# Kernel tuning notes

Hardware: AMD Instinct MI355X
Metric: run time of the kernel (lower is better)

The kernel has to match this reference:

```python
import jax, jax.numpy as jnp
import numpy as np

NUM_EMBEDDINGS = 1024
LATENT_SIZE = 256
N = 131072


def setup_inputs() -> dict:
    key = jax.random.key(0)
    k1, k2 = jax.random.split(key)
    inputs = jax.random.normal(k1, (N, LATENT_SIZE), dtype=jnp.float32)
    embed = jax.random.normal(k2, (LATENT_SIZE, NUM_EMBEDDINGS), dtype=jnp.float32)
    return {"inputs": inputs, "embed": embed}


def reference(inputs, embed):
    # Squared Euclidean distances: [N, K]
    dist = (
        jnp.sum(inputs * inputs, axis=1, keepdims=True)
        - 2.0 * (inputs @ embed)
        + jnp.sum(embed * embed, axis=0, keepdims=True)
    )
    embed_ind = jnp.argmin(dist, axis=1)  # [N]
    embed_onehot = jax.nn.one_hot(embed_ind, NUM_EMBEDDINGS, dtype=inputs.dtype)  # [N, K]
    # Gather codebook vectors: embedding lookup into embed.T -> [N, D]
    quantize = embed.T[embed_ind]
    # Commitment-style loss (eval path: no EMA buffer updates)
    loss = jnp.mean((jax.lax.stop_gradient(quantize) - inputs) ** 2)
    # Straight-through estimator
    quantize = inputs + jax.lax.stop_gradient(quantize - inputs)
    avg_probs = jnp.mean(embed_onehot, axis=0)  # [K]
    perplexity = jnp.exp(-jnp.sum(avg_probs * jnp.log(avg_probs + 1e-10)))
    return quantize, loss, perplexity, embed_ind
```

## Files before the change

kernel.cpp:

```cpp
#include <hip/hip_runtime.h>
#include <math.h>

#define M_ROWS 131072
#define D_DIM 256
#define NCODES 1024
#define QELEMS (M_ROWS * D_DIM)

typedef __attribute__((ext_vector_type(4))) short short4v;
typedef __attribute__((ext_vector_type(8))) short short8v;
typedef __attribute__((ext_vector_type(4))) float f32x4;

#define WS_EMBEDT   0u
#define WS_EHI      1048576u
#define WS_ELO      1572864u
#define WS_ENORM    2097152u
#define WS_PART     2101248u
#define WS_IDX2     18878464u
#define WS_COUNTS   19927040u
#define WS_LOSSP    19931136u

__device__ inline unsigned short f2bf(float x) {
  union { float f; unsigned u; } c; c.f = x;
  unsigned u = c.u;
  u += 0x7FFFu + ((u >> 16) & 1u);
  return (unsigned short)(u >> 16);
}
__device__ inline float bf2f(unsigned short h) {
  union { float f; unsigned u; } c; c.u = ((unsigned)h) << 16;
  return c.f;
}
__device__ inline void merge2(float& b0, int& i0, float& b1, int& i1,
                              float o0, int oi0, float o1, int oi1) {
  if (o0 < b0 || (o0 == b0 && oi0 < i0)) {
    if (b0 < o1 || (b0 == o1 && i0 < oi1)) { b1 = b0; i1 = i0; }
    else { b1 = o1; i1 = oi1; }
    b0 = o0; i0 = oi0;
  } else {
    if (o0 < b1 || (o0 == b1 && oi0 < i1)) { b1 = o0; i1 = oi0; }
  }
}

__global__ __launch_bounds__(256) void k_prep(const float* __restrict__ embed,
                                              float* __restrict__ embedT,
                                              unsigned short* __restrict__ ehiT,
                                              unsigned short* __restrict__ eloT,
                                              float* __restrict__ enorm) {
  int c = blockIdx.x, t = threadIdx.x;
  float v = embed[t * NCODES + c];
  embedT[c * D_DIM + t] = v;
  unsigned short hi = f2bf(v);
  ehiT[c * D_DIM + t] = hi;
  eloT[c * D_DIM + t] = f2bf(v - bf2f(hi));
  float s = v * v;
  for (int off = 32; off > 0; off >>= 1) s += __shfl_down(s, off, 64);
  __shared__ float red[4];
  if ((t & 63) == 0) red[t >> 6] = s;
  __syncthreads();
  if (t == 0) enorm[c] = red[0] + red[1] + red[2] + red[3];
}

__global__ __launch_bounds__(256, 3) void k_dist(const float* __restrict__ A,
                                                 const unsigned short* __restrict__ ehiT,
                                                 const unsigned short* __restrict__ eloT,
                                                 const float* __restrict__ enorm,
                                                 float4* __restrict__ partials) {
  __shared__ unsigned short sAhi[128 * 32];
  __shared__ unsigned short sAlo[128 * 32];
  __shared__ unsigned short sBhi[128 * 32];
  __shared__ unsigned short sBlo[128 * 32];
  __shared__ float4 sRed[2][128];

  int bx = blockIdx.x;
  int ct = bx & 7, rt = bx >> 3;
  int rowBase = rt << 7, colBase = ct << 7;
  int t = threadIdx.x;
  int w = t >> 6, lane = t & 63;
  int wr = w >> 1, wc = w & 1;
  int lm = lane & 15, quad = lane >> 4;

  int sr = t >> 1;
  int skh = (t & 1) << 4;

  f32x4 acc[4][4];
#pragma unroll
  for (int i = 0; i < 4; ++i)
#pragma unroll
    for (int j = 0; j < 4; ++j) acc[i][j] = (f32x4){0.f, 0.f, 0.f, 0.f};

  int aoff[4], boff[4];
#pragma unroll
  for (int ti = 0; ti < 4; ++ti) {
    int r = (wr << 6) + (ti << 4) + lm;
    aoff[ti] = r * 32 + ((quad ^ (r & 3)) << 3);
    int n = (wc << 6) + (ti << 4) + lm;
    boff[ti] = n * 32 + ((quad ^ (n & 3)) << 3);
  }

  const float* Arow = A + (size_t)(rowBase + sr) * D_DIM + skh;
  const unsigned short* Bhirow = ehiT + (size_t)(colBase + sr) * D_DIM + skh;
  const unsigned short* Blorow = eloT + (size_t)(colBase + sr) * D_DIM + skh;

  for (int kc = 0; kc < D_DIM; kc += 32) {
#pragma unroll
    for (int u = 0; u < 4; ++u) {
      float4 v = *(const float4*)(Arow + kc + (u << 2));
      int koff = skh + (u << 2);
      int dst = sr * 32 + (((koff >> 3) ^ (sr & 3)) << 3) + (koff & 7);
      unsigned short h0 = f2bf(v.x), h1 = f2bf(v.y), h2 = f2bf(v.z), h3 = f2bf(v.w);
      short4v hv = {(short)h0, (short)h1, (short)h2, (short)h3};
      *(short4v*)&sAhi[dst] = hv;
      short4v lv = {(short)f2bf(v.x - bf2f(h0)), (short)f2bf(v.y - bf2f(h1)),
                    (short)f2bf(v.z - bf2f(h2)), (short)f2bf(v.w - bf2f(h3))};
      *(short4v*)&sAlo[dst] = lv;
    }
#pragma unroll
    for (int h = 0; h < 2; ++h) {
      int koff = skh + (h << 3);
      int dst = sr * 32 + (((koff >> 3) ^ (sr & 3)) << 3);
      *(uint4*)&sBhi[dst] = *(const uint4*)(Bhirow + kc + (h << 3));
      *(uint4*)&sBlo[dst] = *(const uint4*)(Blorow + kc + (h << 3));
    }
    __syncthreads();

    short8v ahi[4], alo[4], bhi[4], blo[4];
#pragma unroll
    for (int i = 0; i < 4; ++i) {
      ahi[i] = *(const short8v*)&sAhi[aoff[i]];
      bhi[i] = *(const short8v*)&sBhi[boff[i]];
      blo[i] = *(const short8v*)&sBlo[boff[i]];
      alo[i] = *(const short8v*)&sAlo[aoff[i]];
    }
#pragma unroll
    for (int i = 0; i < 4; ++i)
#pragma unroll
      for (int j = 0; j < 4; ++j)
        acc[i][j] = __builtin_amdgcn_mfma_f32_16x16x32_bf16(ahi[i], bhi[j], acc[i][j], 0, 0, 0);
#pragma unroll
    for (int i = 0; i < 4; ++i)
#pragma unroll
      for (int j = 0; j < 4; ++j)
        acc[i][j] = __builtin_amdgcn_mfma_f32_16x16x32_bf16(ahi[i], blo[j], acc[i][j], 0, 0, 0);
#pragma unroll
    for (int i = 0; i < 4; ++i)
#pragma unroll
      for (int j = 0; j < 4; ++j)
        acc[i][j] = __builtin_amdgcn_mfma_f32_16x16x32_bf16(alo[i], bhi[j], acc[i][j], 0, 0, 0);
    __syncthreads();
  }

  float enC[4]; int cidx[4];
#pragma unroll
  for (int j = 0; j < 4; ++j) {
    cidx[j] = colBase + (wc << 6) + (j << 4) + lm;
    enC[j] = enorm[cidx[j]];
  }
#pragma unroll
  for (int ti = 0; ti < 4; ++ti) {
#pragma unroll
    for (int reg = 0; reg < 4; ++reg) {
      float b0 = 3.0e38f, b1 = 3.0e38f;
      int i0 = 0x7fffffff, i1 = 0x7fffffff;
#pragma unroll
      for (int j = 0; j < 4; ++j) {
        float v = fmaf(-2.f, acc[ti][j][reg], enC[j]);
        int c = cidx[j];
        if (v < b0 || (v == b0 && c < i0)) { b1 = b0; i1 = i0; b0 = v; i0 = c; }
        else if (v < b1 || (v == b1 && c < i1)) { b1 = v; i1 = c; }
      }
      for (int m = 1; m < 16; m <<= 1) {
        float o0 = __shfl_xor(b0, m, 64); int oi0 = __shfl_xor(i0, m, 64);
        float o1 = __shfl_xor(b1, m, 64); int oi1 = __shfl_xor(i1, m, 64);
        merge2(b0, i0, b1, i1, o0, oi0, o1, oi1);
      }
      if (lm == 0) {
        int rloc = (wr << 6) + (ti << 4) + (quad << 2) + reg;
        sRed[wc][rloc] = make_float4(b0, (float)i0, b1, (float)i1);
      }
    }
  }
  __syncthreads();
  if (t < 128) {
    float4 p = sRed[0][t];
    float b0 = p.x; int i0 = (int)p.y; float b1 = p.z; int i1 = (int)p.w;
    float4 q = sRed[1][t];
    merge2(b0, i0, b1, i1, q.x, (int)q.y, q.z, (int)q.w);
    partials[(size_t)ct * M_ROWS + rowBase + t] = make_float4(b0, (float)i0, b1, (float)i1);
  }
}

__global__ __launch_bounds__(256) void k_argmin(const float4* __restrict__ partials,
                                                int2* __restrict__ idx2) {
  int row = blockIdx.x * 256 + threadIdx.x;
  float b0 = 3.0e38f, b1 = 3.0e38f;
  int i0 = 0x7fffffff, i1 = 0x7fffffff;
#pragma unroll
  for (int tp = 0; tp < 8; ++tp) {
    float4 p = partials[(size_t)tp * M_ROWS + row];
    merge2(b0, i0, b1, i1, p.x, (int)p.y, p.z, (int)p.w);
  }
  idx2[row] = make_int2(i0, i1);
}

__global__ __launch_bounds__(256) void k_quant(const float* __restrict__ x,
                                               const float* __restrict__ embedT,
                                               const int2* __restrict__ idx2,
                                               float* __restrict__ outq,
                                               float* __restrict__ out_ind,
                                               int* __restrict__ counts,
                                               float* __restrict__ lossPart) {
  int b = blockIdx.x, t = threadIdx.x;
  int rl = t >> 6, lane = t & 63;
  float lsum = 0.f;
  __shared__ float red[4];
#pragma unroll
  for (int ri = 0; ri < 4; ++ri) {
    int row = b * 16 + ri * 4 + rl;
    int2 cc = idx2[row];
    float4 xv = *(const float4*)(x + (size_t)row * D_DIM + (lane << 2));
    float4 q0 = *(const float4*)(embedT + (size_t)cc.x * D_DIM + (lane << 2));
    float4 q1 = *(const float4*)(embedT + (size_t)cc.y * D_DIM + (lane << 2));
    float a0 = q0.x - xv.x, a1 = q0.y - xv.y, a2 = q0.z - xv.z, a3 = q0.w - xv.w;
    float c0 = q1.x - xv.x, c1 = q1.y - xv.y, c2 = q1.z - xv.z, c3 = q1.w - xv.w;
    float d0 = fmaf(a0, a0, fmaf(a1, a1, fmaf(a2, a2, a3 * a3)));
    float d1 = fmaf(c0, c0, fmaf(c1, c1, fmaf(c2, c2, c3 * c3)));
    for (int m = 1; m < 64; m <<= 1) {
      d0 += __shfl_xor(d0, m, 64);
      d1 += __shfl_xor(d1, m, 64);
    }
    bool sel = (d1 < d0) || (d1 == d0 && cc.y < cc.x);
    int widx = sel ? cc.y : cc.x;
    float4 qv;
    qv.x = sel ? q1.x : q0.x; qv.y = sel ? q1.y : q0.y;
    qv.z = sel ? q1.z : q0.z; qv.w = sel ? q1.w : q0.w;
    float4 o = make_float4(xv.x + (qv.x - xv.x), xv.y + (qv.y - xv.y),
                           xv.z + (qv.z - xv.z), xv.w + (qv.w - xv.w));
    *(float4*)(outq + (size_t)row * D_DIM + (lane << 2)) = o;
    lsum += sel ? d1 : d0;
    if (lane == 0) {
      out_ind[row] = (float)widx;
      atomicAdd(&counts[widx], 1);
    }
  }
  if (lane == 0) red[rl] = lsum;
  __syncthreads();
  if (t == 0) lossPart[b] = red[0] + red[1] + red[2] + red[3];
}

__global__ __launch_bounds__(1024) void k_final(const int* __restrict__ counts,
                                                const float* __restrict__ lossPart,
                                                float* __restrict__ out_scalars) {
  int t = threadIdx.x;
  double ls = 0.0;
#pragma unroll
  for (int u = 0; u < 8; ++u) ls += (double)lossPart[t * 8 + u];
  float p = (float)counts[t] * (1.0f / (float)M_ROWS);
  float ent = p * logf(p + 1e-10f);
  double lred = ls;
  float ered = ent;
  for (int off = 32; off > 0; off >>= 1) {
    lred += __shfl_down(lred, off, 64);
    ered += __shfl_down(ered, off, 64);
  }
  __shared__ double lsh[16];
  __shared__ float esh[16];
  int w = t >> 6;
  if ((t & 63) == 0) { lsh[w] = lred; esh[w] = ered; }
  __syncthreads();
  if (t == 0) {
    double L = 0.0;
    float E = 0.f;
    for (int i = 0; i < 16; ++i) { L += lsh[i]; E += esh[i]; }
    out_scalars[0] = (float)(L / (double)QELEMS);
    out_scalars[1] = expf(-E);
  }
}

extern "C" void kernel_launch(void* const* d_in, const int* in_sizes, int n_in,
                              void* d_out, int out_size, void* d_ws, size_t ws_size,
                              hipStream_t stream) {
  const float* inputs = (const float*)d_in[0];
  const float* embed = (const float*)d_in[1];
  float* out = (float*)d_out;
  char* ws = (char*)d_ws;
  float* embedT = (float*)(ws + WS_EMBEDT);
  unsigned short* ehiT = (unsigned short*)(ws + WS_EHI);
  unsigned short* eloT = (unsigned short*)(ws + WS_ELO);
  float* enorm = (float*)(ws + WS_ENORM);
  float4* partials = (float4*)(ws + WS_PART);
  int2* idx2 = (int2*)(ws + WS_IDX2);
  int* counts = (int*)(ws + WS_COUNTS);
  float* lossPart = (float*)(ws + WS_LOSSP);

  hipMemsetAsync(counts, 0, NCODES * sizeof(int), stream);
  k_prep<<<NCODES, 256, 0, stream>>>(embed, embedT, ehiT, eloT, enorm);
  k_dist<<<8192, 256, 0, stream>>>(inputs, ehiT, eloT, enorm, partials);
  k_argmin<<<M_ROWS / 256, 256, 0, stream>>>(partials, idx2);
  k_quant<<<8192, 256, 0, stream>>>(inputs, embedT, idx2, out, out + QELEMS + 2,
                                    counts, lossPart);
  k_final<<<1, 1024, 0, stream>>>(counts, lossPart, out + QELEMS);
}
```

Before: 972.5 us.

## Pre-split inputs to bf16 hi/lo tiles and stream via global_load_lds

Adds a pass that splits the fp32 inputs once into swizzled, tile-contiguous bf16 hi/lo buffers. The embedding split is stored in the same tiled layout, so the distance kernel can copy tiles straight into LDS with global_load_lds instead of redoing the conversion in each of the 8 column-tile blocks per row tile. It also remaps block indices so blocks sharing a row tile land on the same XCD, interleaves LDS fragment loads with MFMA groups, and switches rounding to truncation. This costs an extra pass writing about 134MB of workspace, and it only runs when the workspace is large enough; otherwise the old path is kept.

Measured after the change: 924.3 us. 4.9% less time.

```diff
diff --git a/kernel.cpp b/kernel.cpp
--- a/kernel.cpp
+++ b/kernel.cpp
@@ -6,29 +6,40 @@
 #define NCODES 1024
 #define QELEMS (M_ROWS * D_DIM)
 
-typedef __attribute__((ext_vector_type(4))) short short4v;
 typedef __attribute__((ext_vector_type(8))) short short8v;
 typedef __attribute__((ext_vector_type(4))) float f32x4;
-
-#define WS_EMBEDT   0u
-#define WS_EHI      1048576u
-#define WS_ELO      1572864u
-#define WS_ENORM    2097152u
-#define WS_PART     2101248u
-#define WS_IDX2     18878464u
-#define WS_COUNTS   19927040u
-#define WS_LOSSP    19931136u
-
-__device__ inline unsigned short f2bf(float x) {
-  union { float f; unsigned u; } c; c.f = x;
-  unsigned u = c.u;
-  u += 0x7FFFu + ((u >> 16) & 1u);
-  return (unsigned short)(u >> 16);
-}
-__device__ inline float bf2f(unsigned short h) {
-  union { float f; unsigned u; } c; c.u = ((unsigned)h) << 16;
-  return c.f;
-}
+typedef unsigned short ushort_t;
+
+#define WS_EMBEDT 0u
+#define WS_B1     1048576u
+#define WS_B2     1572864u
+#define WS_ENORM  2097152u
+#define WS_PART   2101248u
+#define WS_IDX2   18878464u
+#define WS_COUNTS 19927040u
+#define WS_LOSSP  19931136u
+#define WS_XHI    19963904u
+#define WS_XLO    87072768u
+#define WS_FAST_TOTAL 154181632u
+
+typedef unsigned int u32_g __attribute__((address_space(1)));
+typedef unsigned int u32_l __attribute__((address_space(3)));
+__device__ inline void gll16(const void* g, void* l) {
+  __builtin_amdgcn_global_load_lds((const u32_g*)g, (u32_l*)l, 16, 0, 0);
+}
+
+__device__ inline unsigned pack2(float x, float y) {
+  return __builtin_amdgcn_perm(__float_as_uint(y), __float_as_uint(x), 0x07060302u);
+}
+__device__ inline float rem1(float x) {
+  return x - __uint_as_float(__float_as_uint(x) & 0xFFFF0000u);
+}
+__device__ inline void split8(float4 a, float4 b, uint4* hi, uint4* lo) {
+  *hi = make_uint4(pack2(a.x, a.y), pack2(a.z, a.w), pack2(b.x, b.y), pack2(b.z, b.w));
+  *lo = make_uint4(pack2(rem1(a.x), rem1(a.y)), pack2(rem1(a.z), rem1(a.w)),
+                   pack2(rem1(b.x), rem1(b.y)), pack2(rem1(b.z), rem1(b.w)));
+}
+
 __device__ inline void merge2(float& b0, int& i0, float& b1, int& i1,
                               float o0, int oi0, float o1, int oi1) {
   if (o0 < b0 || (o0 == b0 && oi0 < i0)) {
@@ -42,15 +53,23 @@
 
 __global__ __launch_bounds__(256) void k_prep(const float* __restrict__ embed,
                                               float* __restrict__ embedT,
-                                              unsigned short* __restrict__ ehiT,
-                                              unsigned short* __restrict__ eloT,
-                                              float* __restrict__ enorm) {
+                                              ushort_t* __restrict__ b1,
+                                              ushort_t* __restrict__ b2,
+                                              float* __restrict__ enorm, int fast) {
   int c = blockIdx.x, t = threadIdx.x;
   float v = embed[t * NCODES + c];
   embedT[c * D_DIM + t] = v;
-  unsigned short hi = f2bf(v);
-  ehiT[c * D_DIM + t] = hi;
-  eloT[c * D_DIM + t] = f2bf(v - bf2f(hi));
+  unsigned bits = __float_as_uint(v);
+  ushort_t hi = (ushort_t)(bits >> 16);
+  ushort_t lo = (ushort_t)(__float_as_uint(rem1(v)) >> 16);
+  if (fast) {
+    int ct = c >> 7, cl = c & 127, kc = t >> 5, u = (t >> 3) & 3, j = t & 7;
+    size_t off = (size_t)(ct * 8 + kc) * 4096 + cl * 32 + ((u ^ (cl & 3)) << 3) + j;
+    b1[off] = hi; b2[off] = lo;
+  } else {
+    b1[c * D_DIM + t] = hi;
+    b2[c * D_DIM + t] = lo;
+  }
   float s = v * v;
   for (int off = 32; off > 0; off >>= 1) s += __shfl_down(s, off, 64);
   __shared__ float red[4];
@@ -59,95 +78,37 @@
   if (t == 0) enorm[c] = red[0] + red[1] + red[2] + red[3];
 }
 
-__global__ __launch_bounds__(256, 3) void k_dist(const float* __restrict__ A,
-                                                 const unsigned short* __restrict__ ehiT,
-                                                 const unsigned short* __restrict__ eloT,
-                                                 const float* __restrict__ enorm,
-                                                 float4* __restrict__ partials) {
-  __shared__ unsigned short sAhi[128 * 32];
-  __shared__ unsigned short sAlo[128 * 32];
-  __shared__ unsigned short sBhi[128 * 32];
-  __shared__ unsigned short sBlo[128 * 32];
-  __shared__ float4 sRed[2][128];
-
-  int bx = blockIdx.x;
-  int ct = bx & 7, rt = bx >> 3;
-  int rowBase = rt << 7, colBase = ct << 7;
-  int t = threadIdx.x;
-  int w = t >> 6, lane = t & 63;
-  int wr = w >> 1, wc = w & 1;
-  int lm = lane & 15, quad = lane >> 4;
-
+__global__ __launch_bounds__(256) void k_asplit(const float* __restrict__ x,
+                                                ushort_t* __restrict__ xhi,
+                                                ushort_t* __restrict__ xlo) {
+  int rt = blockIdx.x, t = threadIdx.x;
   int sr = t >> 1;
-  int skh = (t & 1) << 4;
-
-  f32x4 acc[4][4];
-#pragma unroll
-  for (int i = 0; i < 4; ++i)
-#pragma unroll
-    for (int j = 0; j < 4; ++j) acc[i][j] = (f32x4){0.f, 0.f, 0.f, 0.f};
-
-  int aoff[4], boff[4];
-#pragma unroll
-  for (int ti = 0; ti < 4; ++ti) {
-    int r = (wr << 6) + (ti << 4) + lm;
-    aoff[ti] = r * 32 + ((quad ^ (r & 3)) << 3);
-    int n = (wc << 6) + (ti << 4) + lm;
-    boff[ti] = n * 32 + ((quad ^ (n & 3)) << 3);
-  }
-
-  const float* Arow = A + (size_t)(rowBase + sr) * D_DIM + skh;
-  const unsigned short* Bhirow = ehiT + (size_t)(colBase + sr) * D_DIM + skh;
-  const unsigned short* Blorow = eloT + (size_t)(colBase + sr) * D_DIM + skh;
-
-  for (int kc = 0; kc < D_DIM; kc += 32) {
-#pragma unroll
-    for (int u = 0; u < 4; ++u) {
-      float4 v = *(const float4*)(Arow + kc + (u << 2));
-      int koff = skh + (u << 2);
-      int dst = sr * 32 + (((koff >> 3) ^ (sr & 3)) << 3) + (koff & 7);
-      unsigned short h0 = f2bf(v.x), h1 = f2bf(v.y), h2 = f2bf(v.z), h3 = f2bf(v.w);
-      short4v hv = {(short)h0, (short)h1, (short)h2, (short)h3};
-      *(short4v*)&sAhi[dst] = hv;
-      short4v lv = {(short)f2bf(v.x - bf2f(h0)), (short)f2bf(v.y - bf2f(h1)),
-                    (short)f2bf(v.z - bf2f(h2)), (short)f2bf(v.w - bf2f(h3))};
-      *(short4v*)&sAlo[dst] = lv;
-    }
-#pragma unroll
-    for (int h = 0; h < 2; ++h) {
-      int koff = skh + (h << 3);
-      int dst = sr * 32 + (((koff >> 3) ^ (sr & 3)) << 3);
-      *(uint4*)&sBhi[dst] = *(const uint4*)(Bhirow + kc + (h << 3));
-      *(uint4*)&sBlo[dst] = *(const uint4*)(Blorow + kc + (h << 3));
-    }
-    __syncthreads();
-
-    short8v ahi[4], alo[4], bhi[4], blo[4];
-#pragma unroll
-    for (int i = 0; i < 4; ++i) {
-      ahi[i] = *(const short8v*)&sAhi[aoff[i]];
-      bhi[i] = *(const short8v*)&sBhi[boff[i]];
-      blo[i] = *(const short8v*)&sBlo[boff[i]];
-      alo[i] = *(const short8v*)&sAlo[aoff[i]];
-    }
-#pragma unroll
-    for (int i = 0; i < 4; ++i)
-#pragma unroll
-      for (int j = 0; j < 4; ++j)
-        acc[i][j] = __builtin_amdgcn_mfma_f32_16x16x32_bf16(ahi[i], bhi[j], acc[i][j], 0, 0, 0);
-#pragma unroll
-    for (int i = 0; i < 4; ++i)
-#pragma unroll
-      for (int j = 0; j < 4; ++j)
-        acc[i][j] = __builtin_amdgcn_mfma_f32_16x16x32_bf16(ahi[i], blo[j], acc[i][j], 0, 0, 0);
-#pragma unroll
-    for (int i = 0; i < 4; ++i)
-#pragma unroll
-      for (int j = 0; j < 4; ++j)
-        acc[i][j] = __builtin_amdgcn_mfma_f32_16x16x32_bf16(alo[i], bhi[j], acc[i][j], 0, 0, 0);
-    __syncthreads();
-  }
-
+  int kh = (t & 1) << 4;
+  int s3 = sr & 3;
+  const float* row = x + ((size_t)(rt << 7) + sr) * D_DIM + kh;
+  size_t tb = (size_t)rt * 32768;
+#pragma unroll
+  for (int kc = 0; kc < 8; ++kc) {
+    float4 v0 = *(const float4*)(row + kc * 32 + 0);
+    float4 v1 = *(const float4*)(row + kc * 32 + 4);
+    float4 v2 = *(const float4*)(row + kc * 32 + 8);
+    float4 v3 = *(const float4*)(row + kc * 32 + 12);
+    uint4 h0, l0, h1, l1;
+    split8(v0, v1, &h0, &l0);
+    split8(v2, v3, &h1, &l1);
+    int u0 = kh >> 3;
+    size_t base = tb + (size_t)kc * 4096 + sr * 32;
+    *(uint4*)&xhi[base + ((u0 ^ s3) << 3)] = h0;
+    *(uint4*)&xhi[base + (((u0 + 1) ^ s3) << 3)] = h1;
+    *(uint4*)&xlo[base + ((u0 ^ s3) << 3)] = l0;
+    *(uint4*)&xlo[base + (((u0 + 1) ^ s3) << 3)] = l1;
+  }
+}
+
+__device__ inline void dist_epilogue(f32x4 (&acc)[4][4], const float* __restrict__ enorm,
+                                     float4* __restrict__ partials, float4 (*sRed)[128],
+                                     int t, int wr, int wc, int lm, int quad,
+                                     int rowBase, int colBase, int ct) {
   float enC[4]; int cidx[4];
 #pragma unroll
   for (int j = 0; j < 4; ++j) {
@@ -188,6 +149,176 @@
   }
 }
 
+__global__ __launch_bounds__(256, 3) void k_dist_fast(const ushort_t* __restrict__ xhi,
+                                                      const ushort_t* __restrict__ xlo,
+                                                      const ushort_t* __restrict__ bhi,
+                                                      const ushort_t* __restrict__ blo,
+                                                      const float* __restrict__ enorm,
+                                                      float4* __restrict__ partials) {
+  __shared__ ushort_t sAhi[4096], sAlo[4096], sBhi[4096], sBlo[4096];
+  __shared__ float4 sRed[2][128];
+
+  int bx = blockIdx.x;
+  int xcd = bx & 7, slot = bx >> 3;
+  int rt = (xcd << 7) | (slot >> 3);
+  int ct = slot & 7;
+  int rowBase = rt << 7, colBase = ct << 7;
+  int t = threadIdx.x;
+  int w = t >> 6, lane = t & 63;
+  int wr = w >> 1, wc = w & 1;
+  int lm = lane & 15, quad = lane >> 4;
+
+  f32x4 acc[4][4];
+#pragma unroll
+  for (int i = 0; i < 4; ++i)
+#pragma unroll
+    for (int j = 0; j < 4; ++j) acc[i][j] = (f32x4){0.f, 0.f, 0.f, 0.f};
+
+  int aoff[4], boff[4];
+#pragma unroll
+  for (int ti = 0; ti < 4; ++ti) {
+    int r = (wr << 6) + (ti << 4) + lm;
+    aoff[ti] = r * 32 + ((quad ^ (r & 3)) << 3);
+    int n = (wc << 6) + (ti << 4) + lm;
+    boff[ti] = n * 32 + ((quad ^ (n & 3)) << 3);
+  }
+
+  int c0 = w << 1;
+  int src0 = c0 * 512 + lane * 8;
+  const ushort_t* gA = xhi + (size_t)rt * 32768;
+  const ushort_t* gAl = xlo + (size_t)rt * 32768;
+  const ushort_t* gB = bhi + (size_t)ct * 32768;
+  const ushort_t* gBl = blo + (size_t)ct * 32768;
+
+  for (int kc = 0; kc < 8; ++kc) {
+    int src = kc * 4096 + src0;
+    gll16(gA + src, &sAhi[c0 * 512]);
+    gll16(gA + src + 512, &sAhi[(c0 + 1) * 512]);
+    gll16(gAl + src, &sAlo[c0 * 512]);
+    gll16(gAl + src + 512, &sAlo[(c0 + 1) * 512]);
+    gll16(gB + src, &sBhi[c0 * 512]);
+    gll16(gB + src + 512, &sBhi[(c0 + 1) * 512]);
+    gll16(gBl + src, &sBlo[c0 * 512]);
+    gll16(gBl + src + 512, &sBlo[(c0 + 1) * 512]);
+    __syncthreads();
+
+    short8v ahi[4], bhi_f[4];
+#pragma unroll
+    for (int i = 0; i < 4; ++i) {
+      ahi[i] = *(const short8v*)&sAhi[aoff[i]];
+      bhi_f[i] = *(const short8v*)&sBhi[boff[i]];
+    }
+#pragma unroll
+    for (int i = 0; i < 4; ++i)
+#pragma unroll
+      for (int j = 0; j < 4; ++j)
+        acc[i][j] = __builtin_amdgcn_mfma_f32_16x16x32_bf16(ahi[i], bhi_f[j], acc[i][j], 0, 0, 0);
+    short8v blo_f[4];
+#pragma unroll
+    for (int i = 0; i < 4; ++i) blo_f[i] = *(const short8v*)&sBlo[boff[i]];
+#pragma unroll
+    for (int i = 0; i < 4; ++i)
+#pragma unroll
+      for (int j = 0; j < 4; ++j)
+        acc[i][j] = __builtin_amdgcn_mfma_f32_16x16x32_bf16(ahi[i], blo_f[j], acc[i][j], 0, 0, 0);
+    short8v alo[4];
+#pragma unroll
+    for (int i = 0; i < 4; ++i) alo[i] = *(const short8v*)&sAlo[aoff[i]];
+#pragma unroll
+    for (int i = 0; i < 4; ++i)
+#pragma unroll
+      for (int j = 0; j < 4; ++j)
+        acc[i][j] = __builtin_amdgcn_mfma_f32_16x16x32_bf16(alo[i], bhi_f[j], acc[i][j], 0, 0, 0);
+    __syncthreads();
+  }
+
+  dist_epilogue(acc, enorm, partials, sRed, t, wr, wc, lm, quad, rowBase, colBase, ct);
+}
+
+__global__ __launch_bounds__(256, 3) void k_dist_slow(const float* __restrict__ A,
+                                                      const ushort_t* __restrict__ ehiT,
+                                                      const ushort_t* __restrict__ eloT,
+                                                      const float* __restrict__ enorm,
+                                                      float4* __restrict__ partials) {
+  __shared__ ushort_t sAhi[4096], sAlo[4096], sBhi[4096], sBlo[4096];
+  __shared__ float4 sRed[2][128];
+
+  int bx = blockIdx.x;
+  int ct = bx & 7, rt = bx >> 3;
+  int rowBase = rt << 7, colBase = ct << 7;
+  int t = threadIdx.x;
+  int w = t >> 6, lane = t & 63;
+  int wr = w >> 1, wc = w & 1;
+  int lm = lane & 15, quad = lane >> 4;
+  int sr = t >> 1;
+  int skh = (t & 1) << 4;
+
+  f32x4 acc[4][4];
+#pragma unroll
+  for (int i = 0; i < 4; ++i)
+#pragma unroll
+    for (int j = 0; j < 4; ++j) acc[i][j] = (f32x4){0.f, 0.f, 0.f, 0.f};
+
+  int aoff[4], boff[4];
+#pragma unroll
+  for (int ti = 0; ti < 4; ++ti) {
+    int r = (wr << 6) + (ti << 4) + lm;
+    aoff[ti] = r * 32 + ((quad ^ (r & 3)) << 3);
+    int n = (wc << 6) + (ti << 4) + lm;
+    boff[ti] = n * 32 + ((quad ^ (n & 3)) << 3);
+  }
+
+  const float* Arow = A + (size_t)(rowBase + sr) * D_DIM + skh;
+  const ushort_t* Bhirow = ehiT + (size_t)(colBase + sr) * D_DIM + skh;
+  const ushort_t* Blorow = eloT + (size_t)(colBase + sr) * D_DIM + skh;
+
+  for (int kc = 0; kc < D_DIM; kc += 32) {
+#pragma unroll
+    for (int u = 0; u < 4; ++u) {
+      float4 v = *(const float4*)(Arow + kc + (u << 2));
+      int koff = skh + (u << 2);
+      int dst = sr * 32 + (((koff >> 3) ^ (sr & 3)) << 3) + (koff & 7);
+      *(uint2*)&sAhi[dst] = make_uint2(pack2(v.x, v.y), pack2(v.z, v.w));
+      *(uint2*)&sAlo[dst] = make_uint2(pack2(rem1(v.x), rem1(v.y)), pack2(rem1(v.z), rem1(v.w)));
+    }
+#pragma unroll
+    for (int h = 0; h < 2; ++h) {
+      int koff = skh + (h << 3);
+      int dst = sr * 32 + (((koff >> 3) ^ (sr & 3)) << 3);
+      *(uint4*)&sBhi[dst] = *(const uint4*)(Bhirow + kc + (h << 3));
+      *(uint4*)&sBlo[dst] = *(const uint4*)(Blorow + kc + (h << 3));
+    }
+    __syncthreads();
+
+    short8v ahi[4], bhi_f[4], blo_f[4], alo[4];
+#pragma unroll
+    for (int i = 0; i < 4; ++i) {
+      ahi[i] = *(const short8v*)&sAhi[aoff[i]];
+      bhi_f[i] = *(const short8v*)&sBhi[boff[i]];
+      blo_f[i] = *(const short8v*)&sBlo[boff[i]];
+      alo[i] = *(const short8v*)&sAlo[aoff[i]];
+    }
+#pragma unroll
+    for (int i = 0; i < 4; ++i)
+#pragma unroll
+      for (int j = 0; j < 4; ++j)
+        acc[i][j] = __builtin_amdgcn_mfma_f32_16x16x32_bf16(ahi[i], bhi_f[j], acc[i][j], 0, 0, 0);
+#pragma unroll
+    for (int i = 0; i < 4; ++i)
+#pragma unroll
+      for (int j = 0; j < 4; ++j)
+        acc[i][j] = __builtin_amdgcn_mfma_f32_16x16x32_bf16(ahi[i], blo_f[j], acc[i][j], 0, 0, 0);
+#pragma unroll
+    for (int i = 0; i < 4; ++i)
+#pragma unroll
+      for (int j = 0; j < 4; ++j)
+        acc[i][j] = __builtin_amdgcn_mfma_f32_16x16x32_bf16(alo[i], bhi_f[j], acc[i][j], 0, 0, 0);
+    __syncthreads();
+  }
+
+  dist_epilogue(acc, enorm, partials, sRed, t, wr, wc, lm, quad, rowBase, colBase, ct);
+}
+
 __global__ __launch_bounds__(256) void k_argmin(const float4* __restrict__ partials,
                                                 int2* __restrict__ idx2) {
   int row = blockIdx.x * 256 + threadIdx.x;
@@ -283,17 +414,26 @@
   float* out = (float*)d_out;
   char* ws = (char*)d_ws;
   float* embedT = (float*)(ws + WS_EMBEDT);
-  unsigned short* ehiT = (unsigned short*)(ws + WS_EHI);
-  unsigned short* eloT = (unsigned short*)(ws + WS_ELO);
+  ushort_t* b1 = (ushort_t*)(ws + WS_B1);
+  ushort_t* b2 = (ushort_t*)(ws + WS_B2);
   float* enorm = (float*)(ws + WS_ENORM);
   float4* partials = (float4*)(ws + WS_PART);
   int2* idx2 = (int2*)(ws + WS_IDX2);
   int* counts = (int*)(ws + WS_COUNTS);
   float* lossPart = (float*)(ws + WS_LOSSP);
+  ushort_t* xhi = (ushort_t*)(ws + WS_XHI);
+  ushort_t* xlo = (ushort_t*)(ws + WS_XLO);
+
+  int fast = (ws_size >= (size_t)WS_FAST_TOTAL) ? 1 : 0;
 
   hipMemsetAsync(counts, 0, NCODES * sizeof(int), stream);
-  k_prep<<<NCODES, 256, 0, stream>>>(embed, embedT, ehiT, eloT, enorm);
-  k_dist<<<8192, 256, 0, stream>>>(inputs, ehiT, eloT, enorm, partials);
+  k_prep<<<NCODES, 256, 0, stream>>>(embed, embedT, b1, b2, enorm, fast);
+  if (fast) {
+    k_asplit<<<M_ROWS / 128, 256, 0, stream>>>(inputs, xhi, xlo);
+    k_dist_fast<<<8192, 256, 0, stream>>>(xhi, xlo, b1, b2, enorm, partials);
+  } else {
+    k_dist_slow<<<8192, 256, 0, stream>>>(inputs, b1, b2, enorm, partials);
+  }
   k_argmin<<<M_ROWS / 256, 256, 0, stream>>>(partials, idx2);
   k_quant<<<8192, 256, 0, stream>>>(inputs, embedT, idx2, out, out + QELEMS + 2,
                                     counts, lossPart);
```
